# Kernel tuning notes

Measured on AMD Instinct MI355X. Metric: run time of the kernel, lower is better.

The kernel has to match this reference:

```python
import jax, jax.numpy as jnp
import numpy as np

N_HEADS = 12
EMB_DIM = 768
H_DIM = EMB_DIM // N_HEADS

def setup_inputs() -> dict:
    key = jax.random.key(0)
    ks = jax.random.split(key, 9)
    s = 0.02
    x = jax.random.normal(ks[0], (8, 1024, EMB_DIM), dtype=jnp.float32)
    Wq = jax.random.normal(ks[1], (EMB_DIM, EMB_DIM), dtype=jnp.float32) * s
    Wk = jax.random.normal(ks[2], (EMB_DIM, EMB_DIM), dtype=jnp.float32) * s
    Wv = jax.random.normal(ks[3], (EMB_DIM, EMB_DIM), dtype=jnp.float32) * s
    Wo = jax.random.normal(ks[4], (EMB_DIM, EMB_DIM), dtype=jnp.float32) * s
    bq = jax.random.normal(ks[5], (EMB_DIM,), dtype=jnp.float32) * s
    bk = jax.random.normal(ks[6], (EMB_DIM,), dtype=jnp.float32) * s
    bv = jax.random.normal(ks[7], (EMB_DIM,), dtype=jnp.float32) * s
    bo = jax.random.normal(ks[8], (EMB_DIM,), dtype=jnp.float32) * s
    return {"x": x, "Wq": Wq, "bq": bq, "Wk": Wk, "bk": bk, "Wv": Wv, "bv": bv, "Wo": Wo, "bo": bo}

def reference(x, Wq, bq, Wk, bk, Wv, bv, Wo, bo):
    B, T, E = x.shape
    H, D = N_HEADS, H_DIM
    # projections (torch Linear: y = x @ W^T + b)
    q = (x @ Wq.T + bq).reshape(B, T, H, D).transpose(0, 2, 1, 3)  # [B,H,T,D]
    k = (x @ Wk.T + bk).reshape(B, T, H, D).transpose(0, 2, 1, 3)
    v = (x @ Wv.T + bv).reshape(B, T, H, D).transpose(0, 2, 1, 3)
    scores = jnp.einsum('bhqd,bhkd->bhqk', q, k)  # [B,H,T,T]
    causal = jnp.tril(jnp.ones((T, T), dtype=bool))  # True = keep
    scores = jnp.where(causal, scores, -jnp.inf)
    attn = jax.nn.softmax(scores / jnp.sqrt(jnp.float32(D)), axis=-1)
    # dropout p=0.0 (eval-equivalent): identity
    ctx = jnp.einsum('bhqk,bhkd->bhqd', attn, v)  # [B,H,T,D]
    ctx = ctx.transpose(0, 2, 1, 3).reshape(B, T, E)
    return ctx @ Wo.T + bo
```

## Files before the change

### kernel.cpp

```cpp
#include <hip/hip_runtime.h>
#include <math.h>

typedef unsigned short u16;
typedef __bf16 bf16x8 __attribute__((ext_vector_type(8)));
typedef float f32x4 __attribute__((ext_vector_type(4)));

#define EDIM 768
#define MTOT 8192
#define NH   12
#define HD   64

__device__ __forceinline__ u16 f2bf(float f) {
    __bf16 h = (__bf16)f;
    return __builtin_bit_cast(u16, h);
}

__device__ __forceinline__ void gld_lds16(const u16* g, u16* l) {
    __builtin_amdgcn_global_load_lds(
        (const __attribute__((address_space(1))) void*)g,
        (__attribute__((address_space(3))) void*)l,
        16, 0, 0);
}

__global__ void cvt_kernel(const float* __restrict__ src, u16* __restrict__ dst, int n8) {
    int i = blockIdx.x * blockDim.x + threadIdx.x;
    if (i >= n8) return;
    const float4* s = reinterpret_cast<const float4*>(src) + 2 * (size_t)i;
    float4 v0 = s[0], v1 = s[1];
    union { u16 u[8]; uint4 v; } o;
    o.u[0] = f2bf(v0.x); o.u[1] = f2bf(v0.y); o.u[2] = f2bf(v0.z); o.u[3] = f2bf(v0.w);
    o.u[4] = f2bf(v1.x); o.u[5] = f2bf(v1.y); o.u[6] = f2bf(v1.z); o.u[7] = f2bf(v1.w);
    reinterpret_cast<uint4*>(dst)[i] = o.v;
}

__global__ void cvt4_kernel(const float* __restrict__ s0, const float* __restrict__ s1,
                            const float* __restrict__ s2, const float* __restrict__ s3,
                            u16* __restrict__ dst) {
    int i = blockIdx.x * blockDim.x + threadIdx.x;
    const int m = blockIdx.y;
    const float* src = (m == 0) ? s0 : (m == 1) ? s1 : (m == 2) ? s2 : s3;
    const float4* s = reinterpret_cast<const float4*>(src) + 2 * (size_t)i;
    float4 v0 = s[0], v1 = s[1];
    union { u16 u[8]; uint4 v; } o;
    o.u[0] = f2bf(v0.x); o.u[1] = f2bf(v0.y); o.u[2] = f2bf(v0.z); o.u[3] = f2bf(v0.w);
    o.u[4] = f2bf(v1.x); o.u[5] = f2bf(v1.y); o.u[6] = f2bf(v1.z); o.u[7] = f2bf(v1.w);
    reinterpret_cast<uint4*>(dst + (size_t)m * EDIM * EDIM)[i] = o.v;
}

template<int MODE>
__global__ __launch_bounds__(256) void gemm_bt(
    const u16* __restrict__ A, const u16* __restrict__ Wb,
    const float* __restrict__ bq, const float* __restrict__ bk,
    const float* __restrict__ bv, const float* __restrict__ bo,
    u16* __restrict__ qws, u16* __restrict__ kws, u16* __restrict__ vTws,
    float* __restrict__ out)
{
    __shared__ __align__(16) u16 As[128][32];
    __shared__ __align__(16) u16 Bs[128][32];

    const int tid  = threadIdx.x;
    const int lane = tid & 63, wid = tid >> 6;
    const int g = lane >> 4, c = lane & 15;
    const int wm = wid >> 1, wn = wid & 1;
    const int bm0 = blockIdx.x * 128;
    int mat, nb;
    if (MODE == 0) { mat = blockIdx.y / 6; nb = blockIdx.y % 6; }
    else           { mat = 3;              nb = blockIdx.y; }
    const u16* W = Wb + (size_t)mat * EDIM * EDIM;
    const int bn0 = nb * 128;

    const int srow = wid * 16 + (lane >> 2);
    const int scol = (lane & 3) * 8;

    f32x4 acc[4][4];
    #pragma unroll
    for (int i = 0; i < 4; i++)
        #pragma unroll
        for (int j = 0; j < 4; j++) acc[i][j] = (f32x4){0.f, 0.f, 0.f, 0.f};

    for (int k0 = 0; k0 < EDIM; k0 += 32) {
        __syncthreads();
        #pragma unroll
        for (int rp = 0; rp < 2; ++rp) {
            gld_lds16(&A[(size_t)(bm0 + rp * 64 + srow) * EDIM + k0 + scol],
                      &As[rp * 64 + wid * 16][0]);
            gld_lds16(&W[(size_t)(bn0 + rp * 64 + srow) * EDIM + k0 + scol],
                      &Bs[rp * 64 + wid * 16][0]);
        }
        __syncthreads();

        bf16x8 af[4], bfr[4];
        #pragma unroll
        for (int mi = 0; mi < 4; mi++)
            af[mi] = *reinterpret_cast<const bf16x8*>(&As[wm * 64 + mi * 16 + c][g * 8]);
        #pragma unroll
        for (int ni = 0; ni < 4; ni++)
            bfr[ni] = *reinterpret_cast<const bf16x8*>(&Bs[wn * 64 + ni * 16 + c][g * 8]);
        #pragma unroll
        for (int mi = 0; mi < 4; mi++)
            #pragma unroll
            for (int ni = 0; ni < 4; ni++)
                acc[mi][ni] = __builtin_amdgcn_mfma_f32_16x16x32_bf16(af[mi], bfr[ni], acc[mi][ni], 0, 0, 0);
    }

    #pragma unroll
    for (int mi = 0; mi < 4; mi++) {
        #pragma unroll
        for (int ni = 0; ni < 4; ni++) {
            const int n_in = bn0 + wn * 64 + ni * 16 + c;
            const int m0w  = bm0 + wm * 64 + mi * 16 + g * 4;
            if (MODE == 1) {
                const float bias = bo[n_in];
                #pragma unroll
                for (int r = 0; r < 4; r++)
                    out[(size_t)(m0w + r) * EDIM + n_in] = acc[mi][ni][r] + bias;
            } else {
                const int h = n_in >> 6, d = n_in & 63;
                const int b = m0w >> 10, t = m0w & 1023;
                if (mat == 0) {
                    const float bias = bq[n_in];
                    #pragma unroll
                    for (int r = 0; r < 4; r++)
                        qws[((size_t)(b * NH + h) * 1024 + (t + r)) * HD + d] =
                            f2bf((acc[mi][ni][r] + bias) * 0.180336880f);
                } else if (mat == 1) {
                    const float bias = bk[n_in];
                    #pragma unroll
                    for (int r = 0; r < 4; r++)
                        kws[((size_t)(b * NH + h) * 1024 + (t + r)) * HD + d] =
                            f2bf(acc[mi][ni][r] + bias);
                } else {
                    const float bias = bv[n_in];
                    ushort4 pk;
                    pk.x = f2bf(acc[mi][ni][0] + bias);
                    pk.y = f2bf(acc[mi][ni][1] + bias);
                    pk.z = f2bf(acc[mi][ni][2] + bias);
                    pk.w = f2bf(acc[mi][ni][3] + bias);
                    *reinterpret_cast<ushort4*>(&vTws[((size_t)(b * NH + h) * HD + d) * 1024 + t]) = pk;
                }
            }
        }
    }
}

__global__ __launch_bounds__(256) void attn_kernel(
    const u16* __restrict__ qws, const u16* __restrict__ kws,
    const u16* __restrict__ vTws, u16* __restrict__ ctx)
{
    __shared__ __align__(16) u16 Ks[64][72];
    __shared__ __align__(16) u16 Vs[64][72];
    __shared__ __align__(16) u16 Ps[4][16][72];

    const int tid = threadIdx.x, lane = tid & 63, wid = tid >> 6;
    const int g = lane >> 4, c = lane & 15;
    const int bh = blockIdx.x;
    const int qb = 15 - blockIdx.y;
    const int q0 = qb * 64;
    const u16* Qb = qws + (size_t)bh * 1024 * HD;
    const u16* Kb = kws + (size_t)bh * 1024 * HD;
    const u16* Vb = vTws + (size_t)bh * HD * 1024;

    bf16x8 qf[2];
    const int qrow = q0 + wid * 16 + c;
    #pragma unroll
    for (int kk = 0; kk < 2; kk++)
        qf[kk] = *reinterpret_cast<const bf16x8*>(&Qb[(size_t)qrow * HD + kk * 32 + g * 8]);

    f32x4 o[4];
    #pragma unroll
    for (int df = 0; df < 4; df++) o[df] = (f32x4){0.f, 0.f, 0.f, 0.f};
    float m_run = -INFINITY, l_run = 0.f;

    const int ntiles = qb + 1;
    for (int it = 0; it < ntiles; ++it) {
        const int kv0 = it * 64;
        __syncthreads();
        #pragma unroll
        for (int rp = 0; rp < 2; ++rp) {
            int e = rp * 2048 + tid * 8;
            int row = e >> 6, col = e & 63;
            *reinterpret_cast<uint4*>(&Ks[row][col]) =
                *reinterpret_cast<const uint4*>(&Kb[(size_t)(kv0 + row) * HD + col]);
            *reinterpret_cast<uint4*>(&Vs[row][col]) =
                *reinterpret_cast<const uint4*>(&Vb[(size_t)row * 1024 + kv0 + col]);
        }
        __syncthreads();

        float st[4][4];
        __builtin_amdgcn_s_setprio(1);
        #pragma unroll
        for (int cf = 0; cf < 4; cf++) {
            f32x4 sc = (f32x4){0.f, 0.f, 0.f, 0.f};
            #pragma unroll
            for (int kk = 0; kk < 2; kk++) {
                bf16x8 kb = *reinterpret_cast<const bf16x8*>(&Ks[cf * 16 + c][kk * 32 + g * 8]);
                sc = __builtin_amdgcn_mfma_f32_16x16x32_bf16(kb, qf[kk], sc, 0, 0, 0);
            }
            #pragma unroll
            for (int r = 0; r < 4; r++) st[cf][r] = sc[r];
        }
        __builtin_amdgcn_s_setprio(0);

        if (kv0 == q0) {
            const int q = wid * 16 + c;
            #pragma unroll
            for (int cf = 0; cf < 4; cf++)
                #pragma unroll
                for (int r = 0; r < 4; r++)
                    if (cf * 16 + g * 4 + r > q) st[cf][r] = -INFINITY;
        }

        float tm = st[0][0];
        #pragma unroll
        for (int cf = 0; cf < 4; cf++)
            #pragma unroll
            for (int r = 0; r < 4; r++) tm = fmaxf(tm, st[cf][r]);
        tm = fmaxf(tm, __shfl_xor(tm, 16));
        tm = fmaxf(tm, __shfl_xor(tm, 32));
        const float mn = fmaxf(m_run, tm);
        const float corr = exp2f(m_run - mn);
        float rs = 0.f;
        #pragma unroll
        for (int cf = 0; cf < 4; cf++)
            #pragma unroll
            for (int r = 0; r < 4; r++) {
                const float p = exp2f(st[cf][r] - mn);
                st[cf][r] = p;
                rs += p;
            }
        rs += __shfl_xor(rs, 16);
        rs += __shfl_xor(rs, 32);
        l_run = l_run * corr + rs;
        m_run = mn;

        #pragma unroll
        for (int r = 0; r < 4; r++) {
            const float cr = __shfl(corr, g * 4 + r);
            #pragma unroll
            for (int df = 0; df < 4; df++) o[df][r] *= cr;
        }

        #pragma unroll
        for (int cf = 0; cf < 4; cf++) {
            ushort4 pk;
            pk.x = f2bf(st[cf][0]); pk.y = f2bf(st[cf][1]);
            pk.z = f2bf(st[cf][2]); pk.w = f2bf(st[cf][3]);
            *reinterpret_cast<ushort4*>(&Ps[wid][c][cf * 16 + g * 4]) = pk;
        }
        asm volatile("s_waitcnt lgkmcnt(0)" ::: "memory");
        __builtin_amdgcn_sched_barrier(0);
        bf16x8 pa[2];
        #pragma unroll
        for (int kk = 0; kk < 2; kk++)
            pa[kk] = *reinterpret_cast<const bf16x8*>(&Ps[wid][c][kk * 32 + g * 8]);

        __builtin_amdgcn_s_setprio(1);
        #pragma unroll
        for (int df = 0; df < 4; df++) {
            #pragma unroll
            for (int kk = 0; kk < 2; kk++) {
                bf16x8 vb = *reinterpret_cast<const bf16x8*>(&Vs[df * 16 + c][kk * 32 + g * 8]);
                o[df] = __builtin_amdgcn_mfma_f32_16x16x32_bf16(pa[kk], vb, o[df], 0, 0, 0);
            }
        }
        __builtin_amdgcn_s_setprio(0);
    }

    const int b = bh / NH, h = bh % NH;
    float lb[4];
    #pragma unroll
    for (int r = 0; r < 4; r++) lb[r] = __shfl(l_run, g * 4 + r);
    #pragma unroll
    for (int df = 0; df < 4; df++) {
        #pragma unroll
        for (int r = 0; r < 4; r++) {
            const float val = o[df][r] / lb[r];
            const int t = q0 + wid * 16 + g * 4 + r;
            ctx[((size_t)(b * 1024 + t)) * EDIM + h * HD + df * 16 + c] = f2bf(val);
        }
    }
}

extern "C" void kernel_launch(void* const* d_in, const int* in_sizes, int n_in,
                              void* d_out, int out_size, void* d_ws, size_t ws_size,
                              hipStream_t stream) {
    const float* x  = (const float*)d_in[0];
    const float* Wq = (const float*)d_in[1];
    const float* bq = (const float*)d_in[2];
    const float* Wk = (const float*)d_in[3];
    const float* bk = (const float*)d_in[4];
    const float* Wv = (const float*)d_in[5];
    const float* bv = (const float*)d_in[6];
    const float* Wo = (const float*)d_in[7];
    const float* bo = (const float*)d_in[8];
    float* out = (float*)d_out;

    u16* xb  = (u16*)d_ws;
    u16* wb  = xb  + (size_t)MTOT * EDIM;
    u16* qws = wb  + (size_t)4 * EDIM * EDIM;
    u16* kws = qws + (size_t)MTOT * EDIM;
    u16* vT  = kws + (size_t)MTOT * EDIM;
    u16* ctx = vT  + (size_t)MTOT * EDIM;

    cvt_kernel<<<(MTOT * EDIM / 8 + 255) / 256, 256, 0, stream>>>(x, xb, MTOT * EDIM / 8);
    cvt4_kernel<<<dim3(EDIM * EDIM / 8 / 256, 4), 256, 0, stream>>>(Wq, Wk, Wv, Wo, wb);

    gemm_bt<0><<<dim3(MTOT / 128, 18), 256, 0, stream>>>(xb, wb, bq, bk, bv, bo, qws, kws, vT, nullptr);
    attn_kernel<<<dim3(96, 16), 256, 0, stream>>>(qws, kws, vT, ctx);
    gemm_bt<1><<<dim3(MTOT / 128, 6), 256, 0, stream>>>(ctx, wb, bq, bk, bv, bo, nullptr, nullptr, nullptr, out);
}
```

Baseline: 197.1 us.

## Double-buffer LDS tiles in projection GEMM to overlap loads with MFMA

The projection/output GEMM now keeps two LDS buffers for the A and W tiles and issues the async global-to-LDS loads for the next k-slice before computing on the current one. This halves the barriers per k-step and is meant to hide global load latency behind MFMA work. The cost is double the shared memory (32KB per block), which may reduce occupancy, and the loop is fully unrolled into 12 double-steps.

After: 202.4 us. +2.7%, slower.

```diff
diff --git a/kernel.cpp b/kernel.cpp
--- a/kernel.cpp
+++ b/kernel.cpp
@@ -55,8 +55,8 @@
     u16* __restrict__ qws, u16* __restrict__ kws, u16* __restrict__ vTws,
     float* __restrict__ out)
 {
-    __shared__ __align__(16) u16 As[128][32];
-    __shared__ __align__(16) u16 Bs[128][32];
+    __shared__ __align__(16) u16 As[2][128][32];
+    __shared__ __align__(16) u16 Bs[2][128][32];
 
     const int tid  = threadIdx.x;
     const int lane = tid & 63, wid = tid >> 6;
@@ -71,6 +71,13 @@
 
     const int srow = wid * 16 + (lane >> 2);
     const int scol = (lane & 3) * 8;
+    const u16* gA = A + (size_t)(bm0 + srow) * EDIM + scol;
+    const u16* gB = W + (size_t)(bn0 + srow) * EDIM + scol;
+    const size_t rpo = (size_t)64 * EDIM;
+    u16* lA0 = &As[0][wid * 16][0];  u16* lA0b = &As[0][64 + wid * 16][0];
+    u16* lA1 = &As[1][wid * 16][0];  u16* lA1b = &As[1][64 + wid * 16][0];
+    u16* lB0 = &Bs[0][wid * 16][0];  u16* lB0b = &Bs[0][64 + wid * 16][0];
+    u16* lB1 = &Bs[1][wid * 16][0];  u16* lB1b = &Bs[1][64 + wid * 16][0];
 
     f32x4 acc[4][4];
     #pragma unroll
@@ -78,30 +85,35 @@
         #pragma unroll
         for (int j = 0; j < 4; j++) acc[i][j] = (f32x4){0.f, 0.f, 0.f, 0.f};
 
-    for (int k0 = 0; k0 < EDIM; k0 += 32) {
+    #define STAGE0(k0)  { gld_lds16(gA + (k0), lA0); gld_lds16(gA + rpo + (k0), lA0b); \
+                          gld_lds16(gB + (k0), lB0); gld_lds16(gB + rpo + (k0), lB0b); }
+    #define STAGE1(k0)  { gld_lds16(gA + (k0), lA1); gld_lds16(gA + rpo + (k0), lA1b); \
+                          gld_lds16(gB + (k0), lB1); gld_lds16(gB + rpo + (k0), lB1b); }
+    #define COMPUTE(buf)                                                               \
+        {   bf16x8 af[4], bfr[4];                                                      \
+            _Pragma("unroll") for (int mi = 0; mi < 4; mi++)                           \
+                af[mi] = *reinterpret_cast<const bf16x8*>(&As[buf][wm * 64 + mi * 16 + c][g * 8]); \
+            _Pragma("unroll") for (int ni = 0; ni < 4; ni++)                           \
+                bfr[ni] = *reinterpret_cast<const bf16x8*>(&Bs[buf][wn * 64 + ni * 16 + c][g * 8]); \
+            _Pragma("unroll") for (int mi = 0; mi < 4; mi++)                           \
+                _Pragma("unroll") for (int ni = 0; ni < 4; ni++)                       \
+                    acc[mi][ni] = __builtin_amdgcn_mfma_f32_16x16x32_bf16(af[mi], bfr[ni], acc[mi][ni], 0, 0, 0); }
+
+    STAGE0(0);
+    __syncthreads();
+
+    #pragma unroll
+    for (int t2 = 0; t2 < 12; ++t2) {
+        STAGE1((2 * t2 + 1) * 32);
+        COMPUTE(0);
         __syncthreads();
-        #pragma unroll
-        for (int rp = 0; rp < 2; ++rp) {
-            gld_lds16(&A[(size_t)(bm0 + rp * 64 + srow) * EDIM + k0 + scol],
-                      &As[rp * 64 + wid * 16][0]);
-            gld_lds16(&W[(size_t)(bn0 + rp * 64 + srow) * EDIM + k0 + scol],
-                      &Bs[rp * 64 + wid * 16][0]);
-        }
+        if (t2 < 11) STAGE0((2 * t2 + 2) * 32);
+        COMPUTE(1);
         __syncthreads();
-
-        bf16x8 af[4], bfr[4];
-        #pragma unroll
-        for (int mi = 0; mi < 4; mi++)
-            af[mi] = *reinterpret_cast<const bf16x8*>(&As[wm * 64 + mi * 16 + c][g * 8]);
-        #pragma unroll
-        for (int ni = 0; ni < 4; ni++)
-            bfr[ni] = *reinterpret_cast<const bf16x8*>(&Bs[wn * 64 + ni * 16 + c][g * 8]);
-        #pragma unroll
-        for (int mi = 0; mi < 4; mi++)
-            #pragma unroll
-            for (int ni = 0; ni < 4; ni++)
-                acc[mi][ni] = __builtin_amdgcn_mfma_f32_16x16x32_bf16(af[mi], bfr[ni], acc[mi][ni], 0, 0, 0);
     }
+    #undef STAGE0
+    #undef STAGE1
+    #undef COMPUTE
 
     #pragma unroll
     for (int mi = 0; mi < 4; mi++) {
```
